# Optimization experiments

Measured on AMD Instinct MI355X. Metric: run time of the kernel, lower is better.

The kernel has to match this reference:

```python
import jax, jax.numpy as jnp
import numpy as np

NUM_EMBEDDINGS = 8192
EMBEDDING_DIM = 256


def setup_inputs() -> dict:
    key = jax.random.key(0)
    k1, k2 = jax.random.split(key)
    z = jax.random.normal(k1, (16, EMBEDDING_DIM, 32, 32), dtype=jnp.float32)
    # nn.Embedding default init: N(0, 1)
    emb_table = jax.random.normal(k2, (NUM_EMBEDDINGS, EMBEDDING_DIM), dtype=jnp.float32)
    return {"z": z, "emb_table": emb_table}


def reference(z, emb_table):
    # z: [B, D, H, W]; emb_table: [K, D]
    B, D, H, W = z.shape
    # flatten to per-token vectors: [B*H*W, D]
    zf = z.reshape(B, D, H * W).transpose(0, 2, 1).reshape(B * H * W, D)
    Wt = jax.lax.stop_gradient(emb_table)  # original detaches W for distance
    # argmin of mean squared distance == argmin of squared distance;
    # expand ||z - w||^2 = ||z||^2 - 2 z.w + ||w||^2 (avoid (N,K,D) expansion)
    z_sq = jnp.sum(zf * zf, axis=-1, keepdims=True)          # [N, 1]
    w_sq = jnp.sum(Wt * Wt, axis=-1)                          # [K]
    dists = z_sq - 2.0 * (zf @ Wt.T) + w_sq                   # [N, K]
    token_ids = jnp.argmin(dists, axis=-1)                    # [N]
    quantized = emb_table[token_ids]                          # [N, D] (differentiable gather)
    return quantized.reshape(B, H * W, D).transpose(0, 2, 1).reshape(B, D, H, W)
```

## Files before the change

kernel.cpp:

```cpp
#include <hip/hip_runtime.h>
#include <stdint.h>

#define DIM 256
#define NEMB 8192
#define NTOK 16384
#define HW 1024

typedef __attribute__((ext_vector_type(4))) int int4v;

__device__ __forceinline__ void async_cp16(void* lds, const void* g) {
  __builtin_amdgcn_global_load_lds(
      (const __attribute__((address_space(1))) unsigned int*)g,
      (__attribute__((address_space(3))) unsigned int*)lds, 16, 0, 0);
}
__device__ __forceinline__ int q0_of(float x) {
  int q = __float2int_rn(x * 20.0f);
  return q > 127 ? 127 : (q < -127 ? -127 : q);
}
__device__ __forceinline__ int q1_of(float x, int q0) {
  float e = x * 20.0f - (float)q0;
  int q = __float2int_rn(e * 128.0f);
  return q > 127 ? 127 : (q < -127 ? -127 : q);
}
__device__ __forceinline__ unsigned int pack4(int a, int b, int c, int d) {
  return (unsigned int)(a & 0xff) | ((unsigned int)(b & 0xff) << 8) |
         ((unsigned int)(c & 0xff) << 16) | ((unsigned int)(d & 0xff) << 24);
}
__device__ __forceinline__ void top2_insert(unsigned int v, unsigned int& m1,
                                            unsigned int& m2) {
  unsigned int med;
  asm("v_med3_u32 %0, %1, %2, %3" : "=v"(med) : "v"(v), "v"(m1), "v"(m2));
  m2 = med;
  m1 = v < m1 ? v : m1;
}

__global__ __launch_bounds__(256) void prep_kernel(
    const float* __restrict__ emb, unsigned int* __restrict__ q0w,
    unsigned int* __restrict__ q1w, int* __restrict__ iwsq2,
    const float* __restrict__ z, unsigned int* __restrict__ q0z,
    unsigned int* __restrict__ q1z) {
  __shared__ float tile[64][65];
  int tid = threadIdx.x;
  int lane = tid & 63;
  if (blockIdx.x < 2048) {
    int row = blockIdx.x * 4 + (tid >> 6);
    const float4 v = *(const float4*)(emb + (size_t)row * DIM + lane * 4);
    float s = v.x * v.x + v.y * v.y + v.z * v.z + v.w * v.w;
    int a0 = q0_of(v.x), b0 = q0_of(v.y), c0 = q0_of(v.z), d0 = q0_of(v.w);
    q0w[row * (DIM / 4) + lane] = pack4(a0, b0, c0, d0);
    q1w[row * (DIM / 4) + lane] =
        pack4(q1_of(v.x, a0), q1_of(v.y, b0), q1_of(v.z, c0), q1_of(v.w, d0));
#pragma unroll
    for (int off = 32; off > 0; off >>= 1) s += __shfl_xor(s, off, 64);
    if (lane == 0) iwsq2[row] = (int)rintf(s * 25600.0f) + 8192;
    return;
  }
  int idx = blockIdx.x - 2048;
  int b = idx >> 6, d0 = ((idx >> 4) & 3) * 64, hw0 = (idx & 15) * 64;
  int grp = tid >> 6;
  const float* src = z + (size_t)b * DIM * HW + hw0 + lane;
#pragma unroll
  for (int i = 0; i < 16; i++) {
    int dl = grp + i * 4;
    tile[dl][lane] = src[(size_t)(d0 + dl) * HW];
  }
  __syncthreads();
  int dq = tid & 15;
#pragma unroll
  for (int p = 0; p < 4; p++) {
    int n = (tid >> 4) + p * 16;
    float x0 = tile[dq * 4 + 0][n], x1 = tile[dq * 4 + 1][n];
    float x2 = tile[dq * 4 + 2][n], x3 = tile[dq * 4 + 3][n];
    int a0 = q0_of(x0), b0 = q0_of(x1), c0 = q0_of(x2), e0 = q0_of(x3);
    int token = b * HW + hw0 + n;
    size_t off = (size_t)token * (DIM / 4) + (d0 >> 2) + dq;
    q0z[off] = pack4(a0, b0, c0, e0);
    q1z[off] = pack4(q1_of(x0, a0), q1_of(x1, b0), q1_of(x2, c0), q1_of(x3, e0));
  }
}

__global__ __launch_bounds__(256, 3) void gemm_topk_kernel(
    const signed char* __restrict__ q0z, const signed char* __restrict__ q1z,
    const signed char* __restrict__ q0w, const signed char* __restrict__ q1w,
    const int* __restrict__ iwsq2, uint2* __restrict__ partials) {
  __shared__ __align__(16) signed char sB[2][4][32 * 128];

  const int bid = blockIdx.x;
  const int kq = bid & 7;
  const int tg = bid >> 3;
  const int tid = threadIdx.x;
  const int lane = tid & 63, w = tid >> 6;
  const int c = lane & 15, quad = lane >> 4;
  const int n0 = tg * 128;
  const int k0g = kq * 1024;

  int4v af0[2][4], af1[2][4];
#pragma unroll
  for (int t = 0; t < 2; t++) {
    const size_t arow = (size_t)(n0 + w * 32 + t * 16 + c) * DIM;
#pragma unroll
    for (int s = 0; s < 4; s++) {
      af0[t][s] = *(const int4v*)(q0z + arow + s * 64 + quad * 16);
      af1[t][s] = *(const int4v*)(q1z + arow + s * 64 + quad * 16);
    }
  }

  const int srow = tid >> 3;
  const int scl = ((tid & 7) ^ (srow & 7)) * 16;
  const signed char* p0 = q0w + (size_t)(k0g + srow) * DIM + scl;
  const signed char* p1 = q1w + (size_t)(k0g + srow) * DIM + scl;
  async_cp16(&sB[0][0][tid * 16], p0);
  async_cp16(&sB[0][1][tid * 16], p0 + 128);
  async_cp16(&sB[0][2][tid * 16], p1);
  async_cp16(&sB[0][3][tid * 16], p1 + 128);
  p0 += 32 * DIM;
  p1 += 32 * DIM;
  __syncthreads();

  unsigned int m1[8], m2[8];
#pragma unroll
  for (int i = 0; i < 8; i++) { m1[i] = 0xFFFFFFFFu; m2[i] = 0xFFFFFFFFu; }

  unsigned int idxA = (unsigned)(k0g + c);
  const int4v zero = {0, 0, 0, 0};

  for (int it = 0; it < 32; it++) {
    const int buf = it & 1;
    if (it + 1 < 32) {
      const int nb = buf ^ 1;
      async_cp16(&sB[nb][0][tid * 16], p0);
      async_cp16(&sB[nb][1][tid * 16], p0 + 128);
      async_cp16(&sB[nb][2][tid * 16], p1);
      async_cp16(&sB[nb][3][tid * 16], p1 + 128);
      p0 += 32 * DIM;
      p1 += 32 * DIM;
    }
    const int iw0 = iwsq2[k0g + it * 32 + c];
    const int iw1 = iwsq2[k0g + it * 32 + 16 + c];

    int4v b0a[4], b0b[4];
#pragma unroll
    for (int s = 0; s < 4; s++) {
      const int ph = ((((s & 1) << 2) + quad) ^ (c & 7)) * 16;
      b0a[s] = *(const int4v*)(&sB[buf][s >> 1][c * 128 + ph]);
      b0b[s] = *(const int4v*)(&sB[buf][s >> 1][(16 + c) * 128 + ph]);
    }
    int4v a[2][2];
#pragma unroll
    for (int t = 0; t < 2; t++) {
      a[t][0] = __builtin_amdgcn_mfma_i32_16x16x64_i8(af0[t][0], b0a[0], zero, 0, 0, 0);
      a[t][1] = __builtin_amdgcn_mfma_i32_16x16x64_i8(af0[t][0], b0b[0], zero, 0, 0, 0);
#pragma unroll
      for (int s = 1; s < 4; s++) {
        a[t][0] = __builtin_amdgcn_mfma_i32_16x16x64_i8(af0[t][s], b0a[s], a[t][0], 0, 0, 0);
        a[t][1] = __builtin_amdgcn_mfma_i32_16x16x64_i8(af0[t][s], b0b[s], a[t][1], 0, 0, 0);
      }
    }
#pragma unroll
    for (int t = 0; t < 2; t++)
#pragma unroll
      for (int cn = 0; cn < 2; cn++)
#pragma unroll
        for (int r = 0; r < 4; r++) a[t][cn][r] <<= 7;
#pragma unroll
    for (int t = 0; t < 2; t++)
#pragma unroll
      for (int s = 0; s < 4; s++) {
        a[t][0] = __builtin_amdgcn_mfma_i32_16x16x64_i8(af1[t][s], b0a[s], a[t][0], 0, 0, 0);
        a[t][1] = __builtin_amdgcn_mfma_i32_16x16x64_i8(af1[t][s], b0b[s], a[t][1], 0, 0, 0);
      }
#pragma unroll
    for (int s = 0; s < 4; s++) {
      const int ph = ((((s & 1) << 2) + quad) ^ (c & 7)) * 16;
      int4v b1a = *(const int4v*)(&sB[buf][2 + (s >> 1)][c * 128 + ph]);
      int4v b1b = *(const int4v*)(&sB[buf][2 + (s >> 1)][(16 + c) * 128 + ph]);
#pragma unroll
      for (int t = 0; t < 2; t++) {
        a[t][0] = __builtin_amdgcn_mfma_i32_16x16x64_i8(af0[t][s], b1a, a[t][0], 0, 0, 0);
        a[t][1] = __builtin_amdgcn_mfma_i32_16x16x64_i8(af0[t][s], b1b, a[t][1], 0, 0, 0);
      }
    }
#pragma unroll
    for (int t = 0; t < 2; t++) {
#pragma unroll
      for (int r = 0; r < 4; r++) {
        unsigned int s0 = (unsigned int)(iw0 - a[t][0][r]);
        unsigned int s1 = (unsigned int)(iw1 - a[t][1][r]);
        s0 = s0 < 0x2000000u ? s0 : 0x1FFFFFFu;
        s1 = s1 < 0x2000000u ? s1 : 0x1FFFFFFu;
        unsigned int pk0 = ((s0 << 7) & 0xFFFFE000u) | idxA;
        unsigned int pk1 = ((s1 << 7) & 0xFFFFE000u) | (idxA + 16);
        top2_insert(pk0 < pk1 ? pk0 : pk1, m1[t * 4 + r], m2[t * 4 + r]);
      }
    }
    idxA += 32;
    __syncthreads();
  }

#pragma unroll
  for (int ix = 0; ix < 8; ix++) {
    unsigned int a1m = m1[ix], a2m = m2[ix];
#pragma unroll
    for (int off = 1; off < 16; off <<= 1) {
      unsigned int o1 = __shfl_xor(a1m, off, 16);
      unsigned int o2 = __shfl_xor(a2m, off, 16);
      unsigned int n1 = a1m < o1 ? a1m : o1;
      unsigned int hi = a1m < o1 ? o1 : a1m;
      unsigned int l2 = a2m < o2 ? a2m : o2;
      a2m = hi < l2 ? hi : l2;
      a1m = n1;
    }
    m1[ix] = a1m;
    m2[ix] = a2m;
  }
  if (c == 0) {
#pragma unroll
    for (int t = 0; t < 2; t++) {
#pragma unroll
      for (int r = 0; r < 4; r++) {
        int token = n0 + w * 32 + t * 16 + quad * 4 + r;
        partials[(size_t)kq * NTOK + token] =
            make_uint2(m1[t * 4 + r], m2[t * 4 + r]);
      }
    }
  }
}

__global__ __launch_bounds__(256) void rescore_gather_kernel(
    const uint2* __restrict__ partials, const float* __restrict__ z,
    const float* __restrict__ emb, float* __restrict__ out) {
  __shared__ float tile[32][257];
  __shared__ int sid[32];
  __shared__ int wl[32];
  __shared__ int nwl;
  const int b = blockIdx.x >> 5;
  const int hw0 = (blockIdx.x & 31) * 32;
  const int tid = threadIdx.x;
  if (tid == 0) nwl = 0;
  __syncthreads();
  {
    const int tl = tid >> 3, sub = tid & 7;
    const int token = b * HW + hw0 + tl;
    uint2 e = partials[(size_t)sub * NTOK + token];
    unsigned int m = e.x < e.y ? e.x : e.y;
#pragma unroll
    for (int off = 1; off < 8; off <<= 1) {
      unsigned int o = __shfl_xor(m, off, 8);
      m = o < m ? o : m;
    }
    const unsigned int thr = (m >> 13) + 64;
    int cnt = (((e.x >> 13) <= thr) ? 1 : 0) + (((e.y >> 13) <= thr) ? 1 : 0);
#pragma unroll
    for (int off = 1; off < 8; off <<= 1) cnt += __shfl_xor(cnt, off, 8);
    if (sub == 0) {
      if (cnt == 1) {
        sid[tl] = (int)(m & 0x1FFFu);
      } else {
        int i = atomicAdd(&nwl, 1);
        wl[i] = tl;
      }
    }
  }
  __syncthreads();
  {
    const int w = tid >> 6, lane = tid & 63;
    for (int i = w; i < nwl; i += 4) {
      const int tl = wl[i];
      const int token = b * HW + hw0 + tl;
      unsigned int p[16];
#pragma unroll
      for (int q = 0; q < 8; q++) {
        uint2 t = partials[(size_t)q * NTOK + token];
        p[q * 2] = t.x;
        p[q * 2 + 1] = t.y;
      }
      unsigned int smin = p[0];
#pragma unroll
      for (int q = 1; q < 16; q++) smin = p[q] < smin ? p[q] : smin;
      const unsigned int thr = (smin >> 13) + 64;
      float zv[4];
#pragma unroll
      for (int j = 0; j < 4; j++)
        zv[j] = z[(size_t)b * DIM * HW + (size_t)(lane * 4 + j) * HW + hw0 + tl];
      double best = 1e300;
      int bid2 = NEMB;
#pragma unroll
      for (int q = 0; q < 16; q++) {
        if ((p[q] >> 13) <= thr) {
          int id = (int)(p[q] & 0x1FFFu);
          const float4 wv = *(const float4*)(emb + (size_t)id * DIM + lane * 4);
          double s = (double)wv.x * ((double)wv.x - 2.0 * (double)zv[0]) +
                     (double)wv.y * ((double)wv.y - 2.0 * (double)zv[1]) +
                     (double)wv.z * ((double)wv.z - 2.0 * (double)zv[2]) +
                     (double)wv.w * ((double)wv.w - 2.0 * (double)zv[3]);
#pragma unroll
          for (int off = 32; off > 0; off >>= 1) s += __shfl_xor(s, off, 64);
          if (s < best || (s == best && id < bid2)) {
            best = s;
            bid2 = id;
          }
        }
      }
      if (lane == 0) sid[tl] = bid2;
    }
  }
  __syncthreads();
  for (int i = 0; i < 32; i++)
    tile[i][tid] = emb[(size_t)sid[i] * DIM + tid];
  __syncthreads();
  int h = tid & 31, dg = tid >> 5;
  for (int i = 0; i < 32; i++) {
    int d = i * 8 + dg;
    out[(size_t)b * DIM * HW + (size_t)d * HW + hw0 + h] = tile[h][d];
  }
}

extern "C" void kernel_launch(void* const* d_in, const int* in_sizes, int n_in,
                              void* d_out, int out_size, void* d_ws, size_t ws_size,
                              hipStream_t stream) {
  const float* z = (const float*)d_in[0];
  const float* emb = (const float*)d_in[1];
  float* out = (float*)d_out;
  char* ws = (char*)d_ws;

  signed char* q0w = (signed char*)(ws);
  signed char* q1w = (signed char*)(ws + 2097152);
  signed char* q0z = (signed char*)(ws + 4194304);
  signed char* q1z = (signed char*)(ws + 8388608);
  int* iwsq2 = (int*)(ws + 12582912);
  uint2* partials = (uint2*)(ws + 12615680);

  prep_kernel<<<dim3(3072), 256, 0, stream>>>(
      emb, (unsigned int*)q0w, (unsigned int*)q1w, iwsq2, z, (unsigned int*)q0z,
      (unsigned int*)q1z);
  gemm_topk_kernel<<<dim3(1024), 256, 0, stream>>>(q0z, q1z, q0w, q1w, iwsq2,
                                                   partials);
  rescore_gather_kernel<<<dim3(512), 256, 0, stream>>>(partials, z, emb, out);
}
```

Baseline: 172.6 us.

## Drop z residual quantization term, keep top-3 candidates and widen rescore margin

Removes the second-level int8 residual of z, which drops one quarter of the MFMA work in the distance GEMM along with the q1z prep writes and loads. To make up for the coarser approximate distances, each thread now tracks the three smallest packed scores instead of two. The rescore threshold is widened from 64 to 1536 so more candidates get an exact fp64 rescore. This trades GEMM work for extra top-k bookkeeping, wider partials writes, and possibly more tokens falling into the slow exact-rescore path.

```diff
diff --git a/kernel.cpp b/kernel.cpp
--- a/kernel.cpp
+++ b/kernel.cpp
@@ -26,19 +26,25 @@
   return (unsigned int)(a & 0xff) | ((unsigned int)(b & 0xff) << 8) |
          ((unsigned int)(c & 0xff) << 16) | ((unsigned int)(d & 0xff) << 24);
 }
-__device__ __forceinline__ void top2_insert(unsigned int v, unsigned int& m1,
-                                            unsigned int& m2) {
-  unsigned int med;
-  asm("v_med3_u32 %0, %1, %2, %3" : "=v"(med) : "v"(v), "v"(m1), "v"(m2));
-  m2 = med;
+__device__ __forceinline__ unsigned int med3u(unsigned int a, unsigned int b,
+                                              unsigned int c) {
+  unsigned int m;
+  asm("v_med3_u32 %0, %1, %2, %3" : "=v"(m) : "v"(a), "v"(b), "v"(c));
+  return m;
+}
+__device__ __forceinline__ void top3_insert(unsigned int v, unsigned int& m1,
+                                            unsigned int& m2, unsigned int& m3) {
+  unsigned int t2 = med3u(v, m1, m2);
+  unsigned int t3 = med3u(v, m2, m3);
   m1 = v < m1 ? v : m1;
+  m2 = t2;
+  m3 = t3;
 }
 
 __global__ __launch_bounds__(256) void prep_kernel(
     const float* __restrict__ emb, unsigned int* __restrict__ q0w,
     unsigned int* __restrict__ q1w, int* __restrict__ iwsq2,
-    const float* __restrict__ z, unsigned int* __restrict__ q0z,
-    unsigned int* __restrict__ q1z) {
+    const float* __restrict__ z, unsigned int* __restrict__ q0z) {
   __shared__ float tile[64][65];
   int tid = threadIdx.x;
   int lane = tid & 63;
@@ -69,20 +75,17 @@
 #pragma unroll
   for (int p = 0; p < 4; p++) {
     int n = (tid >> 4) + p * 16;
-    float x0 = tile[dq * 4 + 0][n], x1 = tile[dq * 4 + 1][n];
-    float x2 = tile[dq * 4 + 2][n], x3 = tile[dq * 4 + 3][n];
-    int a0 = q0_of(x0), b0 = q0_of(x1), c0 = q0_of(x2), e0 = q0_of(x3);
+    int a0 = q0_of(tile[dq * 4 + 0][n]), b0 = q0_of(tile[dq * 4 + 1][n]);
+    int c0 = q0_of(tile[dq * 4 + 2][n]), e0 = q0_of(tile[dq * 4 + 3][n]);
     int token = b * HW + hw0 + n;
-    size_t off = (size_t)token * (DIM / 4) + (d0 >> 2) + dq;
-    q0z[off] = pack4(a0, b0, c0, e0);
-    q1z[off] = pack4(q1_of(x0, a0), q1_of(x1, b0), q1_of(x2, c0), q1_of(x3, e0));
+    q0z[(size_t)token * (DIM / 4) + (d0 >> 2) + dq] = pack4(a0, b0, c0, e0);
   }
 }
 
 __global__ __launch_bounds__(256, 3) void gemm_topk_kernel(
-    const signed char* __restrict__ q0z, const signed char* __restrict__ q1z,
-    const signed char* __restrict__ q0w, const signed char* __restrict__ q1w,
-    const int* __restrict__ iwsq2, uint2* __restrict__ partials) {
+    const signed char* __restrict__ q0z, const signed char* __restrict__ q0w,
+    const signed char* __restrict__ q1w, const int* __restrict__ iwsq2,
+    uint4* __restrict__ partials) {
   __shared__ __align__(16) signed char sB[2][4][32 * 128];
 
   const int bid = blockIdx.x;
@@ -94,15 +97,13 @@
   const int n0 = tg * 128;
   const int k0g = kq * 1024;
 
-  int4v af0[2][4], af1[2][4];
+  int4v af0[2][4];
 #pragma unroll
   for (int t = 0; t < 2; t++) {
     const size_t arow = (size_t)(n0 + w * 32 + t * 16 + c) * DIM;
 #pragma unroll
-    for (int s = 0; s < 4; s++) {
+    for (int s = 0; s < 4; s++)
       af0[t][s] = *(const int4v*)(q0z + arow + s * 64 + quad * 16);
-      af1[t][s] = *(const int4v*)(q1z + arow + s * 64 + quad * 16);
-    }
   }
 
   const int srow = tid >> 3;
@@ -117,9 +118,11 @@
   p1 += 32 * DIM;
   __syncthreads();
 
-  unsigned int m1[8], m2[8];
-#pragma unroll
-  for (int i = 0; i < 8; i++) { m1[i] = 0xFFFFFFFFu; m2[i] = 0xFFFFFFFFu; }
+  unsigned int m1[8], m2[8], m3[8];
+#pragma unroll
+  for (int i = 0; i < 8; i++) {
+    m1[i] = 0xFFFFFFFFu; m2[i] = 0xFFFFFFFFu; m3[i] = 0xFFFFFFFFu;
+  }
 
   unsigned int idxA = (unsigned)(k0g + c);
   const int4v zero = {0, 0, 0, 0};
@@ -163,13 +166,6 @@
 #pragma unroll
         for (int r = 0; r < 4; r++) a[t][cn][r] <<= 7;
 #pragma unroll
-    for (int t = 0; t < 2; t++)
-#pragma unroll
-      for (int s = 0; s < 4; s++) {
-        a[t][0] = __builtin_amdgcn_mfma_i32_16x16x64_i8(af1[t][s], b0a[s], a[t][0], 0, 0, 0);
-        a[t][1] = __builtin_amdgcn_mfma_i32_16x16x64_i8(af1[t][s], b0b[s], a[t][1], 0, 0, 0);
-      }
-#pragma unroll
     for (int s = 0; s < 4; s++) {
       const int ph = ((((s & 1) << 2) + quad) ^ (c & 7)) * 16;
       int4v b1a = *(const int4v*)(&sB[buf][2 + (s >> 1)][c * 128 + ph]);
@@ -190,7 +186,8 @@
         s1 = s1 < 0x2000000u ? s1 : 0x1FFFFFFu;
         unsigned int pk0 = ((s0 << 7) & 0xFFFFE000u) | idxA;
         unsigned int pk1 = ((s1 << 7) & 0xFFFFE000u) | (idxA + 16);
-        top2_insert(pk0 < pk1 ? pk0 : pk1, m1[t * 4 + r], m2[t * 4 + r]);
+        top3_insert(pk0 < pk1 ? pk0 : pk1, m1[t * 4 + r], m2[t * 4 + r],
+                    m3[t * 4 + r]);
       }
     }
     idxA += 32;
@@ -199,19 +196,17 @@
 
 #pragma unroll
   for (int ix = 0; ix < 8; ix++) {
-    unsigned int a1m = m1[ix], a2m = m2[ix];
+    unsigned int a1 = m1[ix], a2 = m2[ix], a3 = m3[ix];
 #pragma unroll
     for (int off = 1; off < 16; off <<= 1) {
-      unsigned int o1 = __shfl_xor(a1m, off, 16);
-      unsigned int o2 = __shfl_xor(a2m, off, 16);
-      unsigned int n1 = a1m < o1 ? a1m : o1;
-      unsigned int hi = a1m < o1 ? o1 : a1m;
-      unsigned int l2 = a2m < o2 ? a2m : o2;
-      a2m = hi < l2 ? hi : l2;
-      a1m = n1;
-    }
-    m1[ix] = a1m;
-    m2[ix] = a2m;
+      unsigned int o1 = __shfl_xor(a1, off, 16);
+      unsigned int o2 = __shfl_xor(a2, off, 16);
+      unsigned int o3 = __shfl_xor(a3, off, 16);
+      top3_insert(o1, a1, a2, a3);
+      top3_insert(o2, a1, a2, a3);
+      top3_insert(o3, a1, a2, a3);
+    }
+    m1[ix] = a1; m2[ix] = a2; m3[ix] = a3;
   }
   if (c == 0) {
 #pragma unroll
@@ -220,14 +215,14 @@
       for (int r = 0; r < 4; r++) {
         int token = n0 + w * 32 + t * 16 + quad * 4 + r;
         partials[(size_t)kq * NTOK + token] =
-            make_uint2(m1[t * 4 + r], m2[t * 4 + r]);
+            make_uint4(m1[t * 4 + r], m2[t * 4 + r], m3[t * 4 + r], 0xFFFFFFFFu);
       }
     }
   }
 }
 
 __global__ __launch_bounds__(256) void rescore_gather_kernel(
-    const uint2* __restrict__ partials, const float* __restrict__ z,
+    const uint4* __restrict__ partials, const float* __restrict__ z,
     const float* __restrict__ emb, float* __restrict__ out) {
   __shared__ float tile[32][257];
   __shared__ int sid[32];
@@ -241,15 +236,17 @@
   {
     const int tl = tid >> 3, sub = tid & 7;
     const int token = b * HW + hw0 + tl;
-    uint2 e = partials[(size_t)sub * NTOK + token];
+    uint4 e = partials[(size_t)sub * NTOK + token];
     unsigned int m = e.x < e.y ? e.x : e.y;
+    m = e.z < m ? e.z : m;
 #pragma unroll
     for (int off = 1; off < 8; off <<= 1) {
       unsigned int o = __shfl_xor(m, off, 8);
       m = o < m ? o : m;
     }
-    const unsigned int thr = (m >> 13) + 64;
-    int cnt = (((e.x >> 13) <= thr) ? 1 : 0) + (((e.y >> 13) <= thr) ? 1 : 0);
+    const unsigned int thr = (m >> 13) + 1536;
+    int cnt = (((e.x >> 13) <= thr) ? 1 : 0) + (((e.y >> 13) <= thr) ? 1 : 0) +
+              (((e.z >> 13) <= thr) ? 1 : 0);
 #pragma unroll
     for (int off = 1; off < 8; off <<= 1) cnt += __shfl_xor(cnt, off, 8);
     if (sub == 0) {
@@ -267,17 +264,18 @@
     for (int i = w; i < nwl; i += 4) {
       const int tl = wl[i];
       const int token = b * HW + hw0 + tl;
-      unsigned int p[16];
+      unsigned int p[24];
 #pragma unroll
       for (int q = 0; q < 8; q++) {
-        uint2 t = partials[(size_t)q * NTOK + token];
-        p[q * 2] = t.x;
-        p[q * 2 + 1] = t.y;
+        uint4 t = partials[(size_t)q * NTOK + token];
+        p[q * 3] = t.x;
+        p[q * 3 + 1] = t.y;
+        p[q * 3 + 2] = t.z;
       }
       unsigned int smin = p[0];
 #pragma unroll
-      for (int q = 1; q < 16; q++) smin = p[q] < smin ? p[q] : smin;
-      const unsigned int thr = (smin >> 13) + 64;
+      for (int q = 1; q < 24; q++) smin = p[q] < smin ? p[q] : smin;
+      const unsigned int thr = (smin >> 13) + 1536;
       float zv[4];
 #pragma unroll
       for (int j = 0; j < 4; j++)
@@ -285,7 +283,7 @@
       double best = 1e300;
       int bid2 = NEMB;
 #pragma unroll
-      for (int q = 0; q < 16; q++) {
+      for (int q = 0; q < 24; q++) {
         if ((p[q] >> 13) <= thr) {
           int id = (int)(p[q] & 0x1FFFu);
           const float4 wv = *(const float4*)(emb + (size_t)id * DIM + lane * 4);
@@ -326,14 +324,12 @@
   signed char* q0w = (signed char*)(ws);
   signed char* q1w = (signed char*)(ws + 2097152);
   signed char* q0z = (signed char*)(ws + 4194304);
-  signed char* q1z = (signed char*)(ws + 8388608);
-  int* iwsq2 = (int*)(ws + 12582912);
-  uint2* partials = (uint2*)(ws + 12615680);
+  int* iwsq2 = (int*)(ws + 8388608);
+  uint4* partials = (uint4*)(ws + 8421376);
 
   prep_kernel<<<dim3(3072), 256, 0, stream>>>(
-      emb, (unsigned int*)q0w, (unsigned int*)q1w, iwsq2, z, (unsigned int*)q0z,
-      (unsigned int*)q1z);
-  gemm_topk_kernel<<<dim3(1024), 256, 0, stream>>>(q0z, q1z, q0w, q1w, iwsq2,
+      emb, (unsigned int*)q0w, (unsigned int*)q1w, iwsq2, z, (unsigned int*)q0z);
+  gemm_topk_kernel<<<dim3(1024), 256, 0, stream>>>(q0z, q0w, q1w, iwsq2,
                                                    partials);
   rescore_gather_kernel<<<dim3(512), 256, 0, stream>>>(partials, z, emb, out);
 }
```

Result: faster. 169.0 us (-2.1%).
